# Kernel tuning notes

Measured on AMD Instinct MI355X. Metric: run time of the kernel, lower is better.

Reference implementation:

```python
import jax, jax.numpy as jnp
import numpy as np

B, C, OC, K, HW = 32, 256, 256, 3, 56
M, G = 2, 2
GAP = max(16, C // 16)          # input_gap = 16
MO = M * OC                      # fc1 out channels = 512
FC2_OUT = OC * C * K * K         # 589824
PER = FC2_OUT // MO              # per-group out channels of fc2 = 1152


def setup_inputs() -> dict:
    key = jax.random.key(0)
    ks = jax.random.split(key, 6)
    x = jax.random.normal(ks[0], (B, C, HW, HW), dtype=jnp.float32)
    reduce_w = jax.random.normal(ks[1], (GAP, C), dtype=jnp.float32) / np.sqrt(C)
    reduce_b = jnp.zeros((GAP,), dtype=jnp.float32)
    fc1_w = jax.random.normal(ks[2], (MO, GAP), dtype=jnp.float32) / np.sqrt(GAP)
    # fc2: grouped 1x1 conv, groups=G*OC=512, 1 in-channel per group -> weight (FC2_OUT,)
    fc2_w = jax.random.normal(ks[3], (FC2_OUT,), dtype=jnp.float32)
    fc2_b = jax.random.normal(ks[4], (FC2_OUT,), dtype=jnp.float32) * 0.01
    return {"x": x, "reduce_w": reduce_w, "reduce_b": reduce_b,
            "fc1_w": fc1_w, "fc2_w": fc2_w, "fc2_b": fc2_b}


def reference(x, reduce_w, reduce_b, fc1_w, fc2_w, fc2_b):
    b, c, h, w = x.shape
    # global average pool -> (b, C)
    gap = x.mean(axis=(2, 3))
    # reduce: 1x1 conv on 1x1 map == linear
    g = gap @ reduce_w.T + reduce_b                      # (b, GAP)
    # fc1 (no bias) + sigmoid
    a = jax.nn.sigmoid(g @ fc1_w.T)                      # (b, MO)
    # fc2: grouped 1x1 conv with 1 input channel per group:
    # out[:, g*PER + j] = a[:, g] * fc2_w[g*PER + j] + fc2_b[g*PER + j]
    wk = a[:, :, None] * fc2_w.reshape(MO, PER)[None] + fc2_b.reshape(MO, PER)[None]
    wk = wk.reshape(b * OC, c, K, K)                     # per-sample conv kernels
    pad = K // 2
    y = jax.lax.conv_general_dilated(
        x.reshape(1, b * c, h, w), wk,
        window_strides=(1, 1), padding=[(pad, pad), (pad, pad)],
        feature_group_count=b,
        dimension_numbers=("NCHW", "OIHW", "NCHW"))
    return y.reshape(b, OC, y.shape[2], y.shape[3])
```

## Files before the change

kernel.cpp:

```cpp
#include <hip/hip_runtime.h>
#include <hip/hip_bf16.h>
#include <stdint.h>

#define NB   32
#define NC   256
#define NOC  256
#define HWD  56
#define NPIX 3136
#define PW   58
#define PPIX 3364
#define KTOT 2304
#define MOD  512
#define GAPD 16

#define XBT_BYTES ((size_t)NB * PPIX * NC * 2)
#define WA_BYTES  ((size_t)NB * NOC * KTOT * 2)

typedef __bf16 bf16x8 __attribute__((ext_vector_type(8)));
typedef float  f32x4  __attribute__((ext_vector_type(4)));
typedef unsigned short u16x8 __attribute__((ext_vector_type(8)));

__device__ __forceinline__ unsigned short f2bf(float f) {
    union { float f; unsigned int u; } v; v.f = f;
    unsigned int u = v.u;
    return (unsigned short)((u + 0x7FFFu + ((u >> 16) & 1u)) >> 16);
}

__global__ void se_kernel(const float* __restrict__ gap,
                          const float* __restrict__ rw, const float* __restrict__ rb,
                          const float* __restrict__ f1w, float* __restrict__ a2) {
    __shared__ float sgap[NB * NC];
    __shared__ float sg[NB * GAPD];
    int t = threadIdx.x;
    #pragma unroll
    for (int i = 0; i < 16; ++i) sgap[i * 512 + t] = gap[i * 512 + t];
    __syncthreads();
    {
        int b = t >> 4, tt = t & 15;
        float s = rb[tt];
        for (int c = 0; c < NC; ++c) s += sgap[b * NC + c] * rw[tt * NC + c];
        sg[b * GAPD + tt] = s;
    }
    __syncthreads();
    for (int i = 0; i < 32; ++i) {
        int o = i * 512 + t;
        int b = o >> 9, m = o & 511;
        float s = 0.f;
        #pragma unroll
        for (int tt = 0; tt < GAPD; ++tt) s += sg[b * GAPD + tt] * f1w[m * GAPD + tt];
        a2[o] = 1.0f / (1.0f + __expf(-s));
    }
}

__global__ void wk_kernel(const float* __restrict__ a2,
                          const float* __restrict__ f2w, const float* __restrict__ f2b,
                          unsigned short* __restrict__ wa) {
    __shared__ float sw[KTOT];
    __shared__ float sbv[KTOT];
    __shared__ float sa[2 * NB];
    int oc = blockIdx.x, c = threadIdx.x;
    const float4* wsrc = (const float4*)(f2w + (size_t)oc * KTOT);
    const float4* bsrc = (const float4*)(f2b + (size_t)oc * KTOT);
    #pragma unroll
    for (int i = 0; i < 3; ++i) {
        int idx = i * 256 + c;
        if (idx < 576) {
            ((float4*)sw)[idx] = wsrc[idx];
            ((float4*)sbv)[idx] = bsrc[idx];
        }
    }
    if (c < 64) sa[c] = a2[(c >> 1) * MOD + 2 * oc + (c & 1)];
    __syncthreads();
    float w9[9], b9[9];
    #pragma unroll
    for (int s = 0; s < 9; ++s) { w9[s] = sw[c * 9 + s]; b9[s] = sbv[c * 9 + s]; }
    for (int b = 0; b < NB; ++b) {
        float a0 = sa[2 * b], a1 = sa[2 * b + 1];
        unsigned short* dst = wa + (size_t)(b * NOC + oc) * KTOT;
        #pragma unroll
        for (int s = 0; s < 9; ++s) {
            float a = ((c * 9 + s) >= 1152) ? a1 : a0;
            dst[s * NC + c] = f2bf(a * w9[s] + b9[s]);
        }
    }
}

__global__ void halo_kernel(unsigned short* __restrict__ xbt) {
    int b = blockIdx.x, t = threadIdx.x;
    unsigned short* xb = xbt + (size_t)b * PPIX * NC;
    u16x8 z = {};
    for (int i = t; i < 3712; i += 256) {
        int r = (i >= 1856) ? 1 : 0;
        int c = i - r * 1856;
        int pix = r * (57 * 58) + (c >> 5);
        *(u16x8*)(xb + (size_t)pix * NC + (c & 31) * 8) = z;
    }
    for (int i = t; i < 3584; i += 256) {
        int row = 1 + (i >> 6);
        int side = (i >> 5) & 1;
        int pix = row * PW + side * 57;
        *(u16x8*)(xb + (size_t)pix * NC + (i & 31) * 8) = z;
    }
}

#define TSTR 59
__global__ void xpose_kernel(const float* __restrict__ x, unsigned short* __restrict__ xbt,
                             float* __restrict__ gap) {
    __shared__ unsigned short tile[NC * TSTR];
    int py = blockIdx.x, b = blockIdx.y, t = threadIdx.x;
    int wv = t >> 6, l = t & 63;
    const float* xs = x + (size_t)b * NC * NPIX + py * HWD;
    int q = l & 15;
    int rb4 = l >> 4;
    #pragma unroll
    for (int it = 0; it < 16; ++it) {
        int c = wv * 64 + it * 4 + rb4;
        if (q < 14) {
            float4 v = *(const float4*)(xs + (size_t)c * NPIX + q * 4);
            unsigned short* tr = tile + c * TSTR + q * 4;
            tr[0] = f2bf(v.x); tr[1] = f2bf(v.y); tr[2] = f2bf(v.z); tr[3] = f2bf(v.w);
        }
    }
    __syncthreads();
    {
        float s = 0.f;
        #pragma unroll
        for (int px = 0; px < 56; ++px) {
            union { unsigned int u; float f; } cv;
            cv.u = ((unsigned int)tile[t * TSTR + px]) << 16;
            s += cv.f;
        }
        atomicAdd(&gap[b * NC + t], s * (1.0f / NPIX));
    }
    int cch = t & 31, pg = t >> 5;
    for (int i = 0; i < 7; ++i) {
        int px = pg * 7 + i;
        u16x8 v;
        #pragma unroll
        for (int j = 0; j < 8; ++j) v[j] = tile[(cch * 8 + j) * TSTR + px];
        *(u16x8*)(xbt + ((size_t)b * PPIX + (size_t)(1 + py) * PW + 1 + px) * NC + cch * 8) = v;
    }
}

#define SLICE 24576
#define BOFS  16384

__global__ __launch_bounds__(256, 2) void conv_gemm(
    const unsigned short* __restrict__ wa,
    const unsigned short* __restrict__ xbt,
    float* __restrict__ out)
{
    __shared__ __attribute__((aligned(16))) char lds[3 * SLICE];

    const int bid = blockIdx.x;
    const int wg  = (bid & 7) * 100 + (bid >> 3);
    const int b   = wg / 25, nt = wg % 25;

    const int t = threadIdx.x;
    const int w = t >> 6, l = t & 63;
    const int wm = w >> 1, wn = w & 1;

    const unsigned short* waB = wa + (size_t)b * NOC * KTOT;
    const unsigned short* xbB = xbt + (size_t)b * PPIX * NC;

    const int srow = l >> 2;
    const int sq8  = ((l & 3) ^ ((l >> 3) & 3)) * 8;
    const unsigned short* srcA[4];
    #pragma unroll
    for (int i = 0; i < 4; ++i) {
        int row = (i * 4 + w) * 16 + srow;
        srcA[i] = waB + (size_t)row * KTOT + sq8;
    }
    const unsigned short* srcB[2];
    #pragma unroll
    for (int i = 0; i < 2; ++i) {
        int row = (i * 4 + w) * 16 + srow;
        int pg = nt * 128 + row; if (pg > NPIX - 1) pg = NPIX - 1;
        int py = pg / 56, px = pg - py * 56;
        srcB[i] = xbB + (size_t)((py + 1) * PW + (px + 1)) * NC + sq8;
    }
    const int l16 = l * 16;

    auto issue = [&](int tp, int slot) {
        char* sb = lds + slot * SLICE;
        const int koff = tp * 32;
        const int s9 = tp >> 3;
        const int dy = (s9 >= 6) ? 2 : ((s9 >= 3) ? 1 : 0);
        const int dx = s9 - dy * 3;
        const int bsh = ((dy - 1) * PW + (dx - 1)) * NC + (tp & 7) * 32;
        #pragma unroll
        for (int i = 0; i < 4; ++i)
            __builtin_amdgcn_global_load_lds(
                (const __attribute__((address_space(1))) void*)(srcA[i] + koff),
                (__attribute__((address_space(3))) void*)(sb + (i * 4 + w) * 1024 + l16), 16, 0, 0);
        #pragma unroll
        for (int i = 0; i < 2; ++i)
            __builtin_amdgcn_global_load_lds(
                (const __attribute__((address_space(1))) void*)(srcB[i] + bsh),
                (__attribute__((address_space(3))) void*)(sb + BOFS + (i * 4 + w) * 1024 + l16), 16, 0, 0);
    };

    const int physq16 = (((l >> 4) ^ ((l >> 1) & 3)) << 4);
    const int arow = (l & 15) << 6;

    f32x4 acc[8][4] = {};

    auto compute = [&](int slot) {
        const char* sb = lds + slot * SLICE;
        bf16x8 af[8], bfr[4];
        #pragma unroll
        for (int i = 0; i < 8; ++i)
            af[i] = *(const bf16x8*)(sb + (wm * 8 + i) * 1024 + arow + physq16);
        #pragma unroll
        for (int j = 0; j < 4; ++j)
            bfr[j] = *(const bf16x8*)(sb + BOFS + (wn * 4 + j) * 1024 + arow + physq16);
        __builtin_amdgcn_s_setprio(1);
        #pragma unroll
        for (int i = 0; i < 8; ++i)
            #pragma unroll
            for (int j = 0; j < 4; ++j)
                acc[i][j] = __builtin_amdgcn_mfma_f32_16x16x32_bf16(af[i], bfr[j], acc[i][j], 0, 0, 0);
        __builtin_amdgcn_s_setprio(0);
    };

    issue(0, 0); issue(1, 1);

    int cs = 0;
    for (int p = 0; p < 70; ++p) {
        asm volatile("s_waitcnt vmcnt(6)" ::: "memory");
        __builtin_amdgcn_s_barrier();
        __builtin_amdgcn_sched_barrier(0);
        compute(cs);
        int ns = cs + 2; if (ns >= 3) ns -= 3;
        issue(p + 2, ns);
        ++cs; if (cs == 3) cs = 0;
    }
    asm volatile("s_waitcnt vmcnt(6)" ::: "memory");
    __builtin_amdgcn_s_barrier();
    __builtin_amdgcn_sched_barrier(0);
    compute(cs);
    ++cs; if (cs == 3) cs = 0;
    asm volatile("s_waitcnt vmcnt(0)" ::: "memory");
    __builtin_amdgcn_s_barrier();
    __builtin_amdgcn_sched_barrier(0);
    compute(cs);

    const int ocb = wm * 128 + ((l >> 4) << 2);
    const int pxb = nt * 128 + wn * 64 + (l & 15);
    #pragma unroll
    for (int i = 0; i < 8; ++i) {
        #pragma unroll
        for (int j = 0; j < 4; ++j) {
            int p = pxb + j * 16;
            if (p < NPIX) {
                float* o = out + ((size_t)(b * NOC + ocb + i * 16)) * NPIX + p;
                o[0]        = acc[i][j][0];
                o[NPIX]     = acc[i][j][1];
                o[2 * NPIX] = acc[i][j][2];
                o[3 * NPIX] = acc[i][j][3];
            }
        }
    }
}

extern "C" void kernel_launch(void* const* d_in, const int* in_sizes, int n_in,
                              void* d_out, int out_size, void* d_ws, size_t ws_size,
                              hipStream_t stream) {
    (void)in_sizes; (void)n_in; (void)out_size; (void)ws_size;
    const float* x   = (const float*)d_in[0];
    const float* rw  = (const float*)d_in[1];
    const float* rb  = (const float*)d_in[2];
    const float* f1w = (const float*)d_in[3];
    const float* f2w = (const float*)d_in[4];
    const float* f2b = (const float*)d_in[5];
    float* out = (float*)d_out;

    char* wsb = (char*)d_ws;
    unsigned short* xbt = (unsigned short*)wsb;
    unsigned short* wa  = (unsigned short*)(wsb + XBT_BYTES);
    float* gap = (float*)(wsb + XBT_BYTES + WA_BYTES);
    float* a2  = (float*)(wsb + XBT_BYTES + WA_BYTES + (size_t)NB * NC * 4);

    hipMemsetAsync(gap, 0, (size_t)NB * NC * 4, stream);
    halo_kernel<<<dim3(32), 256, 0, stream>>>(xbt);
    xpose_kernel<<<dim3(56, 32), 256, 0, stream>>>(x, xbt, gap);
    se_kernel<<<dim3(1), 512, 0, stream>>>(gap, rw, rb, f1w, a2);
    wk_kernel<<<dim3(256), 256, 0, stream>>>(a2, f2w, f2b, wa);
    conv_gemm<<<dim3(800), 256, 0, stream>>>(wa, xbt, out);
}
```

Baseline: 210.1 us.

## Retile conv GEMM to 256x224 with 512 threads, fuse SE into weight kernel

The conv GEMM moves from 256 threads with 256x128 tiles and a 3-slot pipeline to 512 threads with 256x224 tiles (14 tiles per batch, exact fit of 3136 pixels) and a 4-slot pipeline, which removes the pixel bounds checks and raises operand reuse per block. The SE MLP is folded into wk_kernel, so each block recomputes the reduce and fc1 stage and the single-block se_kernel launch disappears. The gap memset is moved into halo_kernel. The pool now sums fp32 values through shuffle reductions in xpose instead of summing the bf16 tile. The trade-offs are redundant SE work in 256 blocks, larger LDS use, and more accumulator registers per thread.

```diff
diff --git a/kernel.cpp b/kernel.cpp
--- a/kernel.cpp
+++ b/kernel.cpp
@@ -26,39 +26,28 @@
     return (unsigned short)((u + 0x7FFFu + ((u >> 16) & 1u)) >> 16);
 }
 
-__global__ void se_kernel(const float* __restrict__ gap,
+__global__ void wk_kernel(const float* __restrict__ gap,
                           const float* __restrict__ rw, const float* __restrict__ rb,
-                          const float* __restrict__ f1w, float* __restrict__ a2) {
-    __shared__ float sgap[NB * NC];
-    __shared__ float sg[NB * GAPD];
-    int t = threadIdx.x;
-    #pragma unroll
-    for (int i = 0; i < 16; ++i) sgap[i * 512 + t] = gap[i * 512 + t];
-    __syncthreads();
-    {
-        int b = t >> 4, tt = t & 15;
-        float s = rb[tt];
-        for (int c = 0; c < NC; ++c) s += sgap[b * NC + c] * rw[tt * NC + c];
-        sg[b * GAPD + tt] = s;
-    }
-    __syncthreads();
-    for (int i = 0; i < 32; ++i) {
-        int o = i * 512 + t;
-        int b = o >> 9, m = o & 511;
-        float s = 0.f;
-        #pragma unroll
-        for (int tt = 0; tt < GAPD; ++tt) s += sg[b * GAPD + tt] * f1w[m * GAPD + tt];
-        a2[o] = 1.0f / (1.0f + __expf(-s));
-    }
-}
-
-__global__ void wk_kernel(const float* __restrict__ a2,
+                          const float* __restrict__ f1w,
                           const float* __restrict__ f2w, const float* __restrict__ f2b,
                           unsigned short* __restrict__ wa) {
+    __shared__ float sgap[NB * 257];
+    __shared__ float srw[GAPD * 257];
+    __shared__ float ssg[NB * GAPD];
+    __shared__ float sa[2 * NB];
     __shared__ float sw[KTOT];
     __shared__ float sbv[KTOT];
-    __shared__ float sa[2 * NB];
     int oc = blockIdx.x, c = threadIdx.x;
+    #pragma unroll
+    for (int i = 0; i < 32; ++i) {
+        int idx = i * 256 + c;
+        sgap[(idx >> 8) * 257 + (idx & 255)] = gap[idx];
+    }
+    #pragma unroll
+    for (int i = 0; i < 16; ++i) {
+        int idx = i * 256 + c;
+        srw[(idx >> 8) * 257 + (idx & 255)] = rw[idx];
+    }
     const float4* wsrc = (const float4*)(f2w + (size_t)oc * KTOT);
     const float4* bsrc = (const float4*)(f2b + (size_t)oc * KTOT);
     #pragma unroll
@@ -69,7 +58,24 @@
             ((float4*)sbv)[idx] = bsrc[idx];
         }
     }
-    if (c < 64) sa[c] = a2[(c >> 1) * MOD + 2 * oc + (c & 1)];
+    __syncthreads();
+    #pragma unroll
+    for (int e = 0; e < 2; ++e) {
+        int pair = c * 2 + e;
+        int b = pair >> 4, tt = pair & 15;
+        float s = rb[tt];
+        for (int k = 0; k < NC; ++k) s += sgap[b * 257 + k] * srw[tt * 257 + k];
+        ssg[b * GAPD + tt] = s;
+    }
+    __syncthreads();
+    if (c < 64) {
+        int b = c >> 1, e = c & 1;
+        float s = 0.f;
+        #pragma unroll
+        for (int tt = 0; tt < GAPD; ++tt)
+            s += ssg[b * GAPD + tt] * f1w[(2 * oc + e) * GAPD + tt];
+        sa[c] = 1.0f / (1.0f + __expf(-s));
+    }
     __syncthreads();
     float w9[9], b9[9];
     #pragma unroll
@@ -85,8 +91,9 @@
     }
 }
 
-__global__ void halo_kernel(unsigned short* __restrict__ xbt) {
+__global__ void halo_kernel(unsigned short* __restrict__ xbt, float* __restrict__ gap) {
     int b = blockIdx.x, t = threadIdx.x;
+    gap[b * NC + t] = 0.f;
     unsigned short* xb = xbt + (size_t)b * PPIX * NC;
     u16x8 z = {};
     for (int i = t; i < 3712; i += 256) {
@@ -115,23 +122,20 @@
     #pragma unroll
     for (int it = 0; it < 16; ++it) {
         int c = wv * 64 + it * 4 + rb4;
+        float4 v = {0.f, 0.f, 0.f, 0.f};
         if (q < 14) {
-            float4 v = *(const float4*)(xs + (size_t)c * NPIX + q * 4);
+            v = *(const float4*)(xs + (size_t)c * NPIX + q * 4);
             unsigned short* tr = tile + c * TSTR + q * 4;
             tr[0] = f2bf(v.x); tr[1] = f2bf(v.y); tr[2] = f2bf(v.z); tr[3] = f2bf(v.w);
         }
-    }
-    __syncthreads();
-    {
-        float s = 0.f;
-        #pragma unroll
-        for (int px = 0; px < 56; ++px) {
-            union { unsigned int u; float f; } cv;
-            cv.u = ((unsigned int)tile[t * TSTR + px]) << 16;
-            s += cv.f;
-        }
-        atomicAdd(&gap[b * NC + t], s * (1.0f / NPIX));
-    }
+        float s4 = v.x + v.y + v.z + v.w;
+        s4 += __shfl_xor(s4, 1);
+        s4 += __shfl_xor(s4, 2);
+        s4 += __shfl_xor(s4, 4);
+        s4 += __shfl_xor(s4, 8);
+        if (q == 0) atomicAdd(&gap[b * NC + c], s4 * (1.0f / NPIX));
+    }
+    __syncthreads();
     int cch = t & 31, pg = t >> 5;
     for (int i = 0; i < 7; ++i) {
         int px = pg * 7 + i;
@@ -142,19 +146,22 @@
     }
 }
 
-#define SLICE 24576
+#define SLICE 32768
 #define BOFS  16384
 
-__global__ __launch_bounds__(256, 2) void conv_gemm(
+#define PWAIT(N) do { asm volatile("s_waitcnt vmcnt(" #N ")" ::: "memory"); \
+    __builtin_amdgcn_s_barrier(); __builtin_amdgcn_sched_barrier(0); } while (0)
+
+__global__ __launch_bounds__(512, 2) void conv_gemm(
     const unsigned short* __restrict__ wa,
     const unsigned short* __restrict__ xbt,
     float* __restrict__ out)
 {
-    __shared__ __attribute__((aligned(16))) char lds[3 * SLICE];
+    __shared__ __attribute__((aligned(16))) char lds[4 * SLICE];
 
     const int bid = blockIdx.x;
-    const int wg  = (bid & 7) * 100 + (bid >> 3);
-    const int b   = wg / 25, nt = wg % 25;
+    const int wg  = (bid & 7) * 56 + (bid >> 3);
+    const int b   = wg / 14, nt = wg % 14;
 
     const int t = threadIdx.x;
     const int w = t >> 6, l = t & 63;
@@ -163,23 +170,20 @@
     const unsigned short* waB = wa + (size_t)b * NOC * KTOT;
     const unsigned short* xbB = xbt + (size_t)b * PPIX * NC;
 
-    const int srow = l >> 2;
-    const int sq8  = ((l & 3) ^ ((l >> 3) & 3)) * 8;
-    const unsigned short* srcA[4];
-    #pragma unroll
-    for (int i = 0; i < 4; ++i) {
-        int row = (i * 4 + w) * 16 + srow;
-        srcA[i] = waB + (size_t)row * KTOT + sq8;
-    }
+    const unsigned short* srcA[2];
     const unsigned short* srcB[2];
     #pragma unroll
-    for (int i = 0; i < 2; ++i) {
-        int row = (i * 4 + w) * 16 + srow;
-        int pg = nt * 128 + row; if (pg > NPIX - 1) pg = NPIX - 1;
+    for (int j = 0; j < 2; ++j) {
+        int cix = j * 512 + t;
+        int cc  = cix & 63;
+        int row = (cix >> 6) * 16 + (cc >> 2);
+        int qv  = (cc & 3) ^ ((cc >> 3) & 3);
+        srcA[j] = waB + (size_t)row * KTOT + qv * 8;
+        int pg = nt * 224 + row; if (pg > NPIX - 1) pg = NPIX - 1;
         int py = pg / 56, px = pg - py * 56;
-        srcB[i] = xbB + (size_t)((py + 1) * PW + (px + 1)) * NC + sq8;
-    }
-    const int l16 = l * 16;
+        srcB[j] = xbB + (size_t)((py + 1) * PW + (px + 1)) * NC + qv * 8;
+    }
+    const int t16 = t * 16;
 
     auto issue = [&](int tp, int slot) {
         char* sb = lds + slot * SLICE;
@@ -189,76 +193,62 @@
         const int dx = s9 - dy * 3;
         const int bsh = ((dy - 1) * PW + (dx - 1)) * NC + (tp & 7) * 32;
         #pragma unroll
-        for (int i = 0; i < 4; ++i)
+        for (int j = 0; j < 2; ++j)
             __builtin_amdgcn_global_load_lds(
-                (const __attribute__((address_space(1))) void*)(srcA[i] + koff),
-                (__attribute__((address_space(3))) void*)(sb + (i * 4 + w) * 1024 + l16), 16, 0, 0);
-        #pragma unroll
-        for (int i = 0; i < 2; ++i)
+                (const __attribute__((address_space(1))) void*)(srcA[j] + koff),
+                (__attribute__((address_space(3))) void*)(sb + j * 8192 + t16), 16, 0, 0);
+        #pragma unroll
+        for (int j = 0; j < 2; ++j)
             __builtin_amdgcn_global_load_lds(
-                (const __attribute__((address_space(1))) void*)(srcB[i] + bsh),
-                (__attribute__((address_space(3))) void*)(sb + BOFS + (i * 4 + w) * 1024 + l16), 16, 0, 0);
+                (const __attribute__((address_space(1))) void*)(srcB[j] + bsh),
+                (__attribute__((address_space(3))) void*)(sb + BOFS + j * 8192 + t16), 16, 0, 0);
     };
 
     const int physq16 = (((l >> 4) ^ ((l >> 1) & 3)) << 4);
     const int arow = (l & 15) << 6;
 
-    f32x4 acc[8][4] = {};
+    f32x4 acc[4][7] = {};
 
     auto compute = [&](int slot) {
         const char* sb = lds + slot * SLICE;
-        bf16x8 af[8], bfr[4];
-        #pragma unroll
-        for (int i = 0; i < 8; ++i)
-            af[i] = *(const bf16x8*)(sb + (wm * 8 + i) * 1024 + arow + physq16);
-        #pragma unroll
-        for (int j = 0; j < 4; ++j)
-            bfr[j] = *(const bf16x8*)(sb + BOFS + (wn * 4 + j) * 1024 + arow + physq16);
+        bf16x8 af[4], bfr[7];
+        #pragma unroll
+        for (int m = 0; m < 4; ++m)
+            af[m] = *(const bf16x8*)(sb + (wm * 4 + m) * 1024 + arow + physq16);
+        #pragma unroll
+        for (int j = 0; j < 7; ++j)
+            bfr[j] = *(const bf16x8*)(sb + BOFS + (wn * 7 + j) * 1024 + arow + physq16);
         __builtin_amdgcn_s_setprio(1);
         #pragma unroll
-        for (int i = 0; i < 8; ++i)
+        for (int m = 0; m < 4; ++m)
             #pragma unroll
-            for (int j = 0; j < 4; ++j)
-                acc[i][j] = __builtin_amdgcn_mfma_f32_16x16x32_bf16(af[i], bfr[j], acc[i][j], 0, 0, 0);
+            for (int j = 0; j < 7; ++j)
+                acc[m][j] = __builtin_amdgcn_mfma_f32_16x16x32_bf16(af[m], bfr[j], acc[m][j], 0, 0, 0);
         __builtin_amdgcn_s_setprio(0);
     };
 
     issue(0, 0); issue(1, 1);
 
-    int cs = 0;
+    #pragma unroll 4
     for (int p = 0; p < 70; ++p) {
-        asm volatile("s_waitcnt vmcnt(6)" ::: "memory");
-        __builtin_amdgcn_s_barrier();
-        __builtin_amdgcn_sched_barrier(0);
-        compute(cs);
-        int ns = cs + 2; if (ns >= 3) ns -= 3;
-        issue(p + 2, ns);
-        ++cs; if (cs == 3) cs = 0;
-    }
-    asm volatile("s_waitcnt vmcnt(6)" ::: "memory");
-    __builtin_amdgcn_s_barrier();
-    __builtin_amdgcn_sched_barrier(0);
-    compute(cs);
-    ++cs; if (cs == 3) cs = 0;
-    asm volatile("s_waitcnt vmcnt(0)" ::: "memory");
-    __builtin_amdgcn_s_barrier();
-    __builtin_amdgcn_sched_barrier(0);
-    compute(cs);
-
-    const int ocb = wm * 128 + ((l >> 4) << 2);
-    const int pxb = nt * 128 + wn * 64 + (l & 15);
-    #pragma unroll
-    for (int i = 0; i < 8; ++i) {
-        #pragma unroll
-        for (int j = 0; j < 4; ++j) {
-            int p = pxb + j * 16;
-            if (p < NPIX) {
-                float* o = out + ((size_t)(b * NOC + ocb + i * 16)) * NPIX + p;
-                o[0]        = acc[i][j][0];
-                o[NPIX]     = acc[i][j][1];
-                o[2 * NPIX] = acc[i][j][2];
-                o[3 * NPIX] = acc[i][j][3];
-            }
+        issue(p + 2, (p + 2) & 3);
+        PWAIT(8);
+        compute(p & 3);
+    }
+    PWAIT(4); compute(70 & 3);
+    PWAIT(0); compute(71 & 3);
+
+    const int ocb = wm * 64 + ((l >> 4) << 2);
+    const int pxb = nt * 224 + wn * 112 + (l & 15);
+    #pragma unroll
+    for (int i = 0; i < 4; ++i) {
+        #pragma unroll
+        for (int j = 0; j < 7; ++j) {
+            float* o = out + ((size_t)(b * NOC + ocb + i * 16)) * NPIX + pxb + j * 16;
+            o[0]        = acc[i][j][0];
+            o[NPIX]     = acc[i][j][1];
+            o[2 * NPIX] = acc[i][j][2];
+            o[3 * NPIX] = acc[i][j][3];
         }
     }
 }
@@ -279,12 +269,9 @@
     unsigned short* xbt = (unsigned short*)wsb;
     unsigned short* wa  = (unsigned short*)(wsb + XBT_BYTES);
     float* gap = (float*)(wsb + XBT_BYTES + WA_BYTES);
-    float* a2  = (float*)(wsb + XBT_BYTES + WA_BYTES + (size_t)NB * NC * 4);
-
-    hipMemsetAsync(gap, 0, (size_t)NB * NC * 4, stream);
-    halo_kernel<<<dim3(32), 256, 0, stream>>>(xbt);
+
+    halo_kernel<<<dim3(32), 256, 0, stream>>>(xbt, gap);
     xpose_kernel<<<dim3(56, 32), 256, 0, stream>>>(x, xbt, gap);
-    se_kernel<<<dim3(1), 512, 0, stream>>>(gap, rw, rb, f1w, a2);
-    wk_kernel<<<dim3(256), 256, 0, stream>>>(a2, f2w, f2b, wa);
-    conv_gemm<<<dim3(800), 256, 0, stream>>>(wa, xbt, out);
-}
+    wk_kernel<<<dim3(256), 256, 0, stream>>>(gap, rw, rb, f1w, f2w, f2b, wa);
+    conv_gemm<<<dim3(448), 512, 0, stream>>>(wa, xbt, out);
+}
```

New measurement: 186.1 us. 11.5% less time.
